# Performance work log

Hardware: AMD Instinct MI355X
Metric: run time of the kernel (lower is better)

The kernel has to match this reference:

```python
import jax, jax.numpy as jnp
import numpy as np

B, T, F, H, C = 512, 512, 128, 32, 6

def setup_inputs() -> dict:
    key = jax.random.key(0)
    ks = jax.random.split(key, 6)
    x = jax.random.normal(ks[0], (B, T, F), jnp.float32)
    # random valid lengths; zero-padded tails get masked by Masking(mask_value=0.0)
    lengths = jax.random.randint(ks[1], (B,), T // 4, T + 1)
    tmask = (jnp.arange(T)[None, :] < lengths[:, None]).astype(jnp.float32)
    x = x * tmask[:, :, None]
    Wx = jax.random.normal(ks[2], (F, 4 * H), jnp.float32) / np.sqrt(F).astype(np.float32)
    Wh = jax.random.normal(ks[3], (H, 4 * H), jnp.float32) / np.sqrt(H).astype(np.float32)
    b = jnp.zeros((4 * H,), jnp.float32)
    Wfc = jax.random.normal(ks[4], (H, C), jnp.float32) / np.sqrt(H).astype(np.float32)
    bfc = jnp.zeros((C,), jnp.float32)
    return dict(x=x, Wx=Wx, Wh=Wh, b=b, Wfc=Wfc, bfc=bfc)

def reference(x, Wx, Wh, b, Wfc, bfc):
    # Masking(0.0): timestep masked iff all features == 0
    mask = jnp.any(x != 0.0, axis=-1)                       # [B, T]
    Hh = Wh.shape[0]
    Bn = x.shape[0]
    xt = jnp.transpose(x, (1, 0, 2))                        # [T, B, F]
    mt = jnp.transpose(mask, (1, 0))[:, :, None].astype(x.dtype)  # [T, B, 1]
    # precompute input projection for all steps (one big GEMM)
    xz = jnp.einsum('tbf,fk->tbk', xt, Wx) + b              # [T, B, 4H]

    def step(carry, inp):
        h, c = carry
        zx, m = inp
        z = zx + h @ Wh                                     # [B, 4H]
        i, f, g, o = jnp.split(z, 4, axis=-1)               # keras gate order i,f,c,o
        i = jax.nn.sigmoid(i)
        f = jax.nn.sigmoid(f)
        g = jnp.tanh(g)
        o = jax.nn.sigmoid(o)
        c_new = f * c + i * g
        h_new = o * jnp.tanh(c_new)
        # masked steps keep previous state (Keras masked LSTM semantics)
        h = m * h_new + (1.0 - m) * h
        c = m * c_new + (1.0 - m) * c
        return (h, c), None

    h0 = jnp.zeros((Bn, Hh), x.dtype)
    (h, _), _ = jax.lax.scan(step, (h0, h0), (xz, mt))
    return jax.nn.softmax(h @ Wfc + bfc, axis=-1)           # [B, C]
```

## Files before the change

### kernel.cpp

```cpp
#include <hip/hip_runtime.h>

#define B_ 512
#define T_ 512
#define F_ 128
#define H_ 32
#define C_ 6

typedef float f32x2 __attribute__((ext_vector_type(2)));

__global__ __launch_bounds__(256, 2) void k_xz(
    const float* __restrict__ x, const float* __restrict__ W,
    const float* __restrict__ bias, float* __restrict__ xz,
    float* __restrict__ mask)
{
  __shared__ float xl[128 * 64];
  __shared__ float wl[64 * 128];
  const int tid = threadIdx.x;
  const int m0  = blockIdx.x * 128;
  const int cg  = tid & 15;
  const int rg  = tid >> 4;

  float4 xpre[8], wpre[8];
  int rowbits = 0;

  auto load_chunk = [&](int ch) {
#pragma unroll
    for (int k = 0; k < 8; ++k) {
      const int u = tid + k * 256, r = u >> 4, q = u & 15;
      xpre[k] = *(const float4*)(x + (size_t)(m0 + r) * 128 + ch * 64 + q * 4);
    }
#pragma unroll
    for (int k = 0; k < 8; ++k) {
      const int u = tid + k * 256, f = u >> 5, q = u & 31;
      wpre[k] = *(const float4*)(W + (size_t)(ch * 64 + f) * 128 + q * 4);
    }
  };
  auto mask_chunk = [&]() {
#pragma unroll
    for (int k = 0; k < 8; ++k) {
      const float4 v = xpre[k];
      int nb = ((v.x != 0.f) || (v.y != 0.f) || (v.z != 0.f) || (v.w != 0.f)) ? 1 : 0;
      nb |= __shfl_xor(nb, 1); nb |= __shfl_xor(nb, 2);
      nb |= __shfl_xor(nb, 4); nb |= __shfl_xor(nb, 8);
      rowbits |= nb << k;
    }
  };
  auto write_chunk = [&]() {
#pragma unroll
    for (int k = 0; k < 8; ++k) {
      const int u = tid + k * 256, r = u >> 4, q = u & 15;
      *(float4*)(xl + r * 64 + ((q * 4) ^ (((r >> 3) & 3) << 2))) = xpre[k];
    }
#pragma unroll
    for (int k = 0; k < 8; ++k) {
      const int u = tid + k * 256, f = u >> 5, q = u & 31;
      *(float4*)(wl + f * 128 + q * 4) = wpre[k];
    }
  };

  float acc[8][8];
#pragma unroll
  for (int r = 0; r < 8; ++r)
#pragma unroll
    for (int u = 0; u < 8; ++u) acc[r][u] = 0.f;

  auto compute = [&]() {
#pragma unroll 2
    for (int fq = 0; fq < 16; ++fq) {
      float4 xv[8];
#pragma unroll
      for (int r = 0; r < 8; ++r)
        xv[r] = *(const float4*)(xl + (rg * 8 + r) * 64 + ((fq * 4) ^ ((rg & 3) << 2)));
#pragma unroll
      for (int ff = 0; ff < 4; ++ff) {
        const float* wr = wl + (fq * 4 + ff) * 128 + cg * 4;
        const float4 wa = *(const float4*)(wr);
        const float4 wb = *(const float4*)(wr + 64);
#pragma unroll
        for (int r = 0; r < 8; ++r) {
          const float xs = (ff == 0) ? xv[r].x : (ff == 1) ? xv[r].y
                         : (ff == 2) ? xv[r].z : xv[r].w;
          acc[r][0] += xs * wa.x;  acc[r][1] += xs * wa.y;
          acc[r][2] += xs * wa.z;  acc[r][3] += xs * wa.w;
          acc[r][4] += xs * wb.x;  acc[r][5] += xs * wb.y;
          acc[r][6] += xs * wb.z;  acc[r][7] += xs * wb.w;
        }
      }
    }
  };

  load_chunk(0);
  mask_chunk();
  write_chunk();
  __syncthreads();
  load_chunk(1);
  compute();
  __syncthreads();
  mask_chunk();
  write_chunk();
  __syncthreads();
  compute();

  float bb[8];
#pragma unroll
  for (int u = 0; u < 4; ++u) {
    bb[u]     = bias[cg * 4 + u];
    bb[4 + u] = bias[64 + cg * 4 + u];
  }
#pragma unroll
  for (int r = 0; r < 8; ++r) {
    float* op = xz + (size_t)(m0 + rg * 8 + r) * 128;
    float4 o0 = { acc[r][0] + bb[0], acc[r][1] + bb[1], acc[r][2] + bb[2], acc[r][3] + bb[3] };
    float4 o1 = { acc[r][4] + bb[4], acc[r][5] + bb[5], acc[r][6] + bb[6], acc[r][7] + bb[7] };
    *(float4*)(op + cg * 4)      = o0;
    *(float4*)(op + 64 + cg * 4) = o1;
  }
  if ((tid & 15) == 0) {
#pragma unroll
    for (int k = 0; k < 8; ++k)
      mask[m0 + k * 16 + rg] = (rowbits >> k) & 1 ? 1.f : 0.f;
  }
}

__device__ __forceinline__ float sigmf(float xx) {
  return __builtin_amdgcn_rcpf(1.f + __expf(-xx));
}
__device__ __forceinline__ float tanhf_(float xx) {
  return __builtin_amdgcn_rcpf(1.f + __expf(-2.f * xx)) * 2.f - 1.f;
}

__global__ __launch_bounds__(64, 1) void k_lstm(
    const float* __restrict__ xz, const float* __restrict__ mask,
    const float* __restrict__ Wh, const float* __restrict__ Wfc,
    const float* __restrict__ bfc, float* __restrict__ out)
{
  const int lane = threadIdx.x;
  const int half = lane >> 5;
  const int j = lane & 31;
  const int b = blockIdx.x * 2 + half;

  f32x2 Whr[16][4];
#pragma unroll
  for (int q = 0; q < 16; ++q)
#pragma unroll
    for (int g = 0; g < 4; ++g) {
      Whr[q][g][0] = Wh[(2 * q)     * 128 + g * 32 + j];
      Whr[q][g][1] = Wh[(2 * q + 1) * 128 + g * 32 + j];
    }

  f32x2 hr2[16];
#pragma unroll
  for (int q = 0; q < 16; ++q) { hr2[q][0] = 0.f; hr2[q][1] = 0.f; }
  float cj = 0.f, hj = 0.f;

  __shared__ __align__(16) float hs[2][32];

  const float* xp = xz + (size_t)b * (T_ * 128) + j;
  const float* mp = mask + (size_t)b * T_;

  float xgr[4][4];
  float mr[4];
#pragma unroll
  for (int s = 0; s < 4; ++s) {
#pragma unroll
    for (int g = 0; g < 4; ++g) xgr[s][g] = xp[s * 128 + g * 32];
    mr[s] = mp[s];
  }

  for (int t0 = 0; t0 < T_; t0 += 4) {
#pragma unroll
    for (int s = 0; s < 4; ++s) {
      const int t = t0 + s;
      f32x2 a[4];
#pragma unroll
      for (int g = 0; g < 4; ++g) { a[g][0] = xgr[s][g]; a[g][1] = 0.f; }
      const float m = mr[s];

      int pf = t + 4;
      if (pf > T_ - 1) pf = T_ - 1;
#pragma unroll
      for (int g = 0; g < 4; ++g) xgr[s][g] = xp[(size_t)pf * 128 + g * 32];
      mr[s] = mp[pf];

#pragma unroll
      for (int q = 0; q < 16; ++q) {
#pragma unroll
        for (int g = 0; g < 4; ++g)
          asm("v_pk_fma_f32 %0, %1, %2, %0" : "+v"(a[g]) : "v"(hr2[q]), "v"(Whr[q][g]));
      }
      const float zi = a[0][0] + a[0][1];
      const float zf = a[1][0] + a[1][1];
      const float zg = a[2][0] + a[2][1];
      const float zo = a[3][0] + a[3][1];

      const float ig = sigmf(zi);
      const float fg = sigmf(zf);
      const float gg = tanhf_(zg);
      const float og = sigmf(zo);
      const float cn = fg * cj + ig * gg;
      const float hn = og * tanhf_(cn);
      cj += m * (cn - cj);
      hj += m * (hn - hj);

      hs[half][j] = hj;
      __syncthreads();
#pragma unroll
      for (int q = 0; q < 8; ++q) {
        const float4 v = *(const float4*)(&hs[half][q * 4]);
        hr2[2 * q][0]     = v.x; hr2[2 * q][1]     = v.y;
        hr2[2 * q + 1][0] = v.z; hr2[2 * q + 1][1] = v.w;
      }
    }
  }

  float hrs[32];
#pragma unroll
  for (int q = 0; q < 16; ++q) { hrs[2 * q] = hr2[q][0]; hrs[2 * q + 1] = hr2[q][1]; }
  float logits[C_];
#pragma unroll
  for (int c = 0; c < C_; ++c) {
    float aa = bfc[c];
#pragma unroll
    for (int f = 0; f < 32; ++f) aa += hrs[f] * Wfc[f * C_ + c];
    logits[c] = aa;
  }
  if (j == 0) {
    float mx = logits[0];
#pragma unroll
    for (int c = 1; c < C_; ++c) mx = fmaxf(mx, logits[c]);
    float e[C_], s = 0.f;
#pragma unroll
    for (int c = 0; c < C_; ++c) { e[c] = __expf(logits[c] - mx); s += e[c]; }
    const float rs = 1.f / s;
#pragma unroll
    for (int c = 0; c < C_; ++c) out[(size_t)b * C_ + c] = e[c] * rs;
  }
}

extern "C" void kernel_launch(void* const* d_in, const int* in_sizes, int n_in,
                              void* d_out, int out_size, void* d_ws, size_t ws_size,
                              hipStream_t stream) {
  const float* x   = (const float*)d_in[0];
  const float* Wx  = (const float*)d_in[1];
  const float* Wh  = (const float*)d_in[2];
  const float* bv  = (const float*)d_in[3];
  const float* Wfc = (const float*)d_in[4];
  const float* bfc = (const float*)d_in[5];
  float* out = (float*)d_out;

  float* xz   = (float*)d_ws;
  float* mask = (float*)((char*)d_ws + (size_t)B_ * T_ * 128 * 4);

  k_xz<<<(B_ * T_) / 128, 256, 0, stream>>>(x, Wx, bv, xz, mask);
  k_lstm<<<B_ / 2, 64, 0, stream>>>(xz, mask, Wh, Wfc, bfc, out);
}
```

Baseline: 298.7 us.

## Split LSTM gate columns across wave halves and broadcast h via readlane

The recurrent kernel now assigns one batch row per 64-lane wave. Each lane computes two gate columns instead of four, and the lane halves trade partial gates with a cross-half shuffle. The hidden-state broadcast through shared memory and `__syncthreads` is replaced by 32 readlanes into scalar registers, which takes the LDS round trip and barrier off the sequential critical path. In exchange, the grid doubles to one wave per batch row, the packed FMA is dropped for scalar FMAs, and a shuffle is added every step.

```diff
diff --git a/kernel.cpp b/kernel.cpp
--- a/kernel.cpp
+++ b/kernel.cpp
@@ -5,8 +5,6 @@
 #define F_ 128
 #define H_ 32
 #define C_ 6
-
-typedef float f32x2 __attribute__((ext_vector_type(2)));
 
 __global__ __launch_bounds__(256, 2) void k_xz(
     const float* __restrict__ x, const float* __restrict__ W,
@@ -136,34 +134,33 @@
 {
   const int lane = threadIdx.x;
   const int half = lane >> 5;
-  const int j = lane & 31;
-  const int b = blockIdx.x * 2 + half;
-
-  f32x2 Whr[16][4];
-#pragma unroll
-  for (int q = 0; q < 16; ++q)
-#pragma unroll
-    for (int g = 0; g < 4; ++g) {
-      Whr[q][g][0] = Wh[(2 * q)     * 128 + g * 32 + j];
-      Whr[q][g][1] = Wh[(2 * q + 1) * 128 + g * 32 + j];
-    }
-
-  f32x2 hr2[16];
-#pragma unroll
-  for (int q = 0; q < 16; ++q) { hr2[q][0] = 0.f; hr2[q][1] = 0.f; }
+  const int j    = lane & 31;
+  const int b    = blockIdx.x;
+
+  const int colA = half * 32 + j;
+  const int colB = 64 + half * 32 + j;
+
+  float WhA[32], WhB[32];
+#pragma unroll
+  for (int f = 0; f < 32; ++f) {
+    WhA[f] = Wh[f * 128 + colA];
+    WhB[f] = Wh[f * 128 + colB];
+  }
+
+  float hsc[32];
+#pragma unroll
+  for (int f = 0; f < 32; ++f) hsc[f] = 0.f;
+
   float cj = 0.f, hj = 0.f;
 
-  __shared__ __align__(16) float hs[2][32];
-
-  const float* xp = xz + (size_t)b * (T_ * 128) + j;
-  const float* mp = mask + (size_t)b * T_;
-
-  float xgr[4][4];
-  float mr[4];
+  const float* xrow = xz + (size_t)b * (T_ * 128);
+  const float* mp   = mask + (size_t)b * T_;
+
+  float xa[4], xb[4], mr[4];
 #pragma unroll
   for (int s = 0; s < 4; ++s) {
-#pragma unroll
-    for (int g = 0; g < 4; ++g) xgr[s][g] = xp[s * 128 + g * 32];
+    xa[s] = xrow[s * 128 + colA];
+    xb[s] = xrow[s * 128 + colB];
     mr[s] = mp[s];
   }
 
@@ -171,27 +168,31 @@
 #pragma unroll
     for (int s = 0; s < 4; ++s) {
       const int t = t0 + s;
-      f32x2 a[4];
-#pragma unroll
-      for (int g = 0; g < 4; ++g) { a[g][0] = xgr[s][g]; a[g][1] = 0.f; }
+      float zA0 = xa[s], zA1 = 0.f;
+      float zB0 = xb[s], zB1 = 0.f;
       const float m = mr[s];
 
       int pf = t + 4;
       if (pf > T_ - 1) pf = T_ - 1;
-#pragma unroll
-      for (int g = 0; g < 4; ++g) xgr[s][g] = xp[(size_t)pf * 128 + g * 32];
+      xa[s] = xrow[(size_t)pf * 128 + colA];
+      xb[s] = xrow[(size_t)pf * 128 + colB];
       mr[s] = mp[pf];
 
 #pragma unroll
-      for (int q = 0; q < 16; ++q) {
-#pragma unroll
-        for (int g = 0; g < 4; ++g)
-          asm("v_pk_fma_f32 %0, %1, %2, %0" : "+v"(a[g]) : "v"(hr2[q]), "v"(Whr[q][g]));
+      for (int f = 0; f < 16; ++f) {
+        zA0 += hsc[2 * f]     * WhA[2 * f];
+        zA1 += hsc[2 * f + 1] * WhA[2 * f + 1];
+        zB0 += hsc[2 * f]     * WhB[2 * f];
+        zB1 += hsc[2 * f + 1] * WhB[2 * f + 1];
       }
-      const float zi = a[0][0] + a[0][1];
-      const float zf = a[1][0] + a[1][1];
-      const float zg = a[2][0] + a[2][1];
-      const float zo = a[3][0] + a[3][1];
+      const float zA = zA0 + zA1;
+      const float zB = zB0 + zB1;
+      const float oA = __shfl_xor(zA, 32);
+      const float oB = __shfl_xor(zB, 32);
+      const float zi = half ? oA : zA;
+      const float zf = half ? zA : oA;
+      const float zg = half ? oB : zB;
+      const float zo = half ? zB : oB;
 
       const float ig = sigmf(zi);
       const float fg = sigmf(zf);
@@ -202,36 +203,28 @@
       cj += m * (cn - cj);
       hj += m * (hn - hj);
 
-      hs[half][j] = hj;
-      __syncthreads();
-#pragma unroll
-      for (int q = 0; q < 8; ++q) {
-        const float4 v = *(const float4*)(&hs[half][q * 4]);
-        hr2[2 * q][0]     = v.x; hr2[2 * q][1]     = v.y;
-        hr2[2 * q + 1][0] = v.z; hr2[2 * q + 1][1] = v.w;
-      }
-    }
-  }
-
-  float hrs[32];
-#pragma unroll
-  for (int q = 0; q < 16; ++q) { hrs[2 * q] = hr2[q][0]; hrs[2 * q + 1] = hr2[q][1]; }
+#pragma unroll
+      for (int f = 0; f < 32; ++f)
+        hsc[f] = __uint_as_float(__builtin_amdgcn_readlane(__float_as_uint(hj), f));
+    }
+  }
+
   float logits[C_];
 #pragma unroll
   for (int c = 0; c < C_; ++c) {
     float aa = bfc[c];
 #pragma unroll
-    for (int f = 0; f < 32; ++f) aa += hrs[f] * Wfc[f * C_ + c];
+    for (int f = 0; f < 32; ++f) aa += hsc[f] * Wfc[f * C_ + c];
     logits[c] = aa;
   }
-  if (j == 0) {
+  if (lane == 0) {
     float mx = logits[0];
 #pragma unroll
     for (int c = 1; c < C_; ++c) mx = fmaxf(mx, logits[c]);
-    float e[C_], s = 0.f;
-#pragma unroll
-    for (int c = 0; c < C_; ++c) { e[c] = __expf(logits[c] - mx); s += e[c]; }
-    const float rs = 1.f / s;
+    float e[C_], sden = 0.f;
+#pragma unroll
+    for (int c = 0; c < C_; ++c) { e[c] = __expf(logits[c] - mx); sden += e[c]; }
+    const float rs = 1.f / sden;
 #pragma unroll
     for (int c = 0; c < C_; ++c) out[(size_t)b * C_ + c] = e[c] * rs;
   }
@@ -252,5 +245,5 @@
   float* mask = (float*)((char*)d_ws + (size_t)B_ * T_ * 128 * 4);
 
   k_xz<<<(B_ * T_) / 128, 256, 0, stream>>>(x, Wx, bv, xz, mask);
-  k_lstm<<<B_ / 2, 64, 0, stream>>>(xz, mask, Wh, Wfc, bfc, out);
-}
+  k_lstm<<<B_, 64, 0, stream>>>(xz, mask, Wh, Wfc, bfc, out);
+}
```

Result: faster. 271.3 us (-9.2%).
